# Kernel tuning notes

Hardware: AMD Instinct MI355X
Metric: run time of the kernel (lower is better)

## Reference

```python
import jax, jax.numpy as jnp
import numpy as np

B, S, D, H = 2, 2048, 1024, 16
HD = D // H  # head_dim = 64


def setup_inputs() -> dict:
    key = jax.random.key(0)
    ks = jax.random.split(key, 11)
    sc = 1.0 / np.sqrt(D)
    inp = {
        "query": jax.random.normal(ks[0], (B, S, D), jnp.float32),
        "key_": jax.random.normal(ks[1], (B, S, D), jnp.float32),
        "value": jax.random.normal(ks[2], (B, S, D), jnp.float32),
        "Wq": jax.random.normal(ks[3], (D, D), jnp.float32) * sc,
        "bq": jnp.zeros((D,), jnp.float32),
        "Wk": jax.random.normal(ks[4], (D, D), jnp.float32) * sc,
        "bk": jnp.zeros((D,), jnp.float32),
        "Wv": jax.random.normal(ks[5], (D, D), jnp.float32) * sc,
        "bv": jnp.zeros((D,), jnp.float32),
        "Wo": jax.random.normal(ks[6], (D, D), jnp.float32) * sc,
        "bo": jnp.zeros((D,), jnp.float32),
    }
    return inp


def _split_heads(x):
    # [B,S,D] -> [B,H,S,HD]
    return x.reshape(B, -1, H, HD).transpose(0, 2, 1, 3)


def reference(query, key_, value, Wq, bq, Wk, bk, Wv, bv, Wo, bo):
    q = _split_heads(query @ Wq.T + bq)
    k = _split_heads(key_ @ Wk.T + bk)
    v = _split_heads(value @ Wv.T + bv)
    scores = jnp.einsum("bhqd,bhkd->bhqk", q, k) / jnp.sqrt(jnp.float32(HD))
    attn = jax.nn.softmax(scores, axis=-1)  # dropout is identity in eval
    out = jnp.einsum("bhqk,bhkd->bhqd", attn, v)
    out = out.transpose(0, 2, 1, 3).reshape(B, -1, D)
    return out @ Wo.T + bo
```

## Files before the change

### kernel.cpp

```cpp
#include <hip/hip_runtime.h>
#include <hip/hip_bf16.h>
#include <stdint.h>

#define B_  2
#define S_  2048
#define D_  1024
#define H_  16
#define HD_ 64
#define M_  (B_*S_)

typedef __bf16 bf16x8 __attribute__((ext_vector_type(8)));
typedef __bf16 bf16x4 __attribute__((ext_vector_type(4)));
typedef short  s16x4  __attribute__((ext_vector_type(4)));
typedef float  f32x4  __attribute__((ext_vector_type(4)));
typedef unsigned int u32x4 __attribute__((ext_vector_type(4)));
typedef unsigned int u32x2 __attribute__((ext_vector_type(2)));
typedef unsigned short ushort_t;
typedef ushort_t u16x8 __attribute__((ext_vector_type(8)));

#define LOG2E 1.44269504088896f

#if __has_builtin(__builtin_amdgcn_exp2f)
#define EXP2(x) __builtin_amdgcn_exp2f(x)
#else
#define EXP2(x) exp2f(x)
#endif

__device__ __forceinline__ ushort_t f2bf(float f) {
    return __builtin_bit_cast(ushort_t, (__bf16)f);
}
__device__ __forceinline__ bf16x8 load_frag(const ushort_t* p) {
    u32x4 r = *reinterpret_cast<const u32x4*>(p);
    return __builtin_bit_cast(bf16x8, r);
}
__device__ __forceinline__ bf16x8 lds_frag(const ushort_t* p) {
    u32x4 r = *reinterpret_cast<const u32x4*>(p);
    return __builtin_bit_cast(bf16x8, r);
}
__device__ __forceinline__ bf16x4 lds_frag4(const ushort_t* p) {
    u32x2 r = *reinterpret_cast<const u32x2*>(p);
    return __builtin_bit_cast(bf16x4, r);
}
__device__ __forceinline__ void gld_lds16(const ushort_t* g, ushort_t* l) {
    __builtin_amdgcn_global_load_lds(
        (const __attribute__((address_space(1))) void*)g,
        (__attribute__((address_space(3))) void*)l, 16, 0, 0);
}

__device__ __forceinline__ f32x4 mfma16_bf16(bf16x4 a, bf16x4 b, f32x4 c) {
#if __has_builtin(__builtin_amdgcn_mfma_f32_16x16x16_bf16)
    return __builtin_amdgcn_mfma_f32_16x16x16_bf16(a, b, c, 0, 0, 0);
#elif __has_builtin(__builtin_amdgcn_mfma_f32_16x16x16bf16_1k)
    return __builtin_amdgcn_mfma_f32_16x16x16bf16_1k(
        __builtin_bit_cast(s16x4, a), __builtin_bit_cast(s16x4, b), c, 0, 0, 0);
#else
    f32x4 d;
    asm("v_mfma_f32_16x16x16_bf16 %0, %1, %2, %3"
        : "=v"(d) : "v"(a), "v"(b), "v"(c));
    return d;
#endif
}

__device__ __forceinline__ void cvt_body(const float* __restrict__ in,
                                         ushort_t* __restrict__ out, int i) {
    f32x4 v0 = *reinterpret_cast<const f32x4*>(in + i);
    f32x4 v1 = *reinterpret_cast<const f32x4*>(in + i + 4);
    u16x8 o;
#pragma unroll
    for (int j = 0; j < 4; ++j) { o[j] = f2bf(v0[j]); o[4 + j] = f2bf(v1[j]); }
    *reinterpret_cast<u16x8*>(out + i) = o;
}

__global__ __launch_bounds__(256) void cvt_all_kernel(
    const float* q, const float* k, const float* v,
    const float* fwq, const float* fwk, const float* fwv, const float* fwo,
    ushort_t* oq, ushort_t* ok, ushort_t* ov,
    ushort_t* owq, ushort_t* owk, ushort_t* owv, ushort_t* owo)
{
    const size_t T = (size_t)M_ * D_;
    const size_t U = (size_t)D_ * D_;
    const size_t idx = ((size_t)blockIdx.x * 256 + threadIdx.x) * 8;
    const float* in; ushort_t* out; size_t off;
    if (idx < 3 * T) {
        const size_t w = idx >> 22; off = idx & (T - 1);
        in  = (w == 0) ? q  : (w == 1) ? k  : v;
        out = (w == 0) ? oq : (w == 1) ? ok : ov;
    } else {
        const size_t r = idx - 3 * T;
        const size_t w = r >> 20; off = r & (U - 1);
        in  = (w == 0) ? fwq : (w == 1) ? fwk : (w == 2) ? fwv : fwo;
        out = (w == 0) ? owq : (w == 1) ? owk : (w == 2) ? owv : owo;
    }
    cvt_body(in, out, (int)off);
}

__device__ __forceinline__ void gemm_body(const ushort_t* __restrict__ X,
                                          const ushort_t* __restrict__ W,
                                          const float* __restrict__ bias,
                                          void* __restrict__ out, int mode)
{
    __shared__ ushort_t lA[128 * 32];
    __shared__ ushort_t lB[128 * 32];

    const int tid  = threadIdx.x;
    const int lane = tid & 63;
    const int wv   = tid >> 6;
    const int m0   = blockIdx.x * 128;
    const int n0   = blockIdx.y * 128;
    const int wr   = (wv >> 1) * 64;
    const int wc   = (wv & 1) * 64;
    const int l15  = lane & 15;
    const int lg   = lane >> 4;

    f32x4 acc[4][4];
#pragma unroll
    for (int i = 0; i < 4; ++i)
#pragma unroll
        for (int j = 0; j < 4; ++j) acc[i][j] = (f32x4){0.f, 0.f, 0.f, 0.f};

    const int srow = lane >> 2;
    const int skc  = ((lane & 3) ^ ((srow >> 1) & 3)) * 8;
    const int c0   = wv * 2, c1 = wv * 2 + 1;
    const size_t arow0 = (size_t)(m0 + c0 * 16 + srow) * D_ + skc;
    const size_t arow1 = (size_t)(m0 + c1 * 16 + srow) * D_ + skc;
    const size_t brow0 = (size_t)(n0 + c0 * 16 + srow) * D_ + skc;
    const size_t brow1 = (size_t)(n0 + c1 * 16 + srow) * D_ + skc;

    const int rchunk = (lg ^ ((l15 >> 1) & 3)) * 8;

    for (int kt = 0; kt < D_ / 32; ++kt) {
        const int k0 = kt * 32;
        gld_lds16(X + arow0 + k0, &lA[c0 * 512]);
        gld_lds16(X + arow1 + k0, &lA[c1 * 512]);
        gld_lds16(W + brow0 + k0, &lB[c0 * 512]);
        gld_lds16(W + brow1 + k0, &lB[c1 * 512]);
        __syncthreads();

        bf16x8 a[4], b[4];
#pragma unroll
        for (int i = 0; i < 4; ++i)
            a[i] = lds_frag(&lA[(wr + i * 16 + l15) * 32 + rchunk]);
#pragma unroll
        for (int j = 0; j < 4; ++j)
            b[j] = lds_frag(&lB[(wc + j * 16 + l15) * 32 + rchunk]);
#pragma unroll
        for (int i = 0; i < 4; ++i)
#pragma unroll
            for (int j = 0; j < 4; ++j)
                acc[i][j] = __builtin_amdgcn_mfma_f32_16x16x32_bf16(a[i], b[j], acc[i][j], 0, 0, 0);
        __syncthreads();
    }

#pragma unroll
    for (int i = 0; i < 4; ++i) {
#pragma unroll
        for (int j = 0; j < 4; ++j) {
            const int gcol = n0 + wc + j * 16 + l15;
            const float bv = bias[gcol];
#pragma unroll
            for (int r = 0; r < 4; ++r) {
                const int grow = m0 + wr + i * 16 + lg * 4 + r;
                float v = acc[i][j][r] + bv;
                if (mode == 0) v *= 0.125f * LOG2E;
                if (mode == 3) {
                    ((float*)out)[(size_t)grow * D_ + gcol] = v;
                } else {
                    const int b = grow >> 11, s = grow & (S_ - 1);
                    const int h = gcol >> 6,  hd = gcol & 63;
                    size_t addr;
                    if (mode == 2) addr = ((size_t)(b * H_ + h) * HD_ + hd) * S_ + s;
                    else           addr = ((size_t)(b * H_ + h) * S_ + s) * HD_ + hd;
                    ((ushort_t*)out)[addr] = f2bf(v);
                }
            }
        }
    }
}

__global__ __launch_bounds__(256) void qkv_kernel(
    const ushort_t* q_in, const ushort_t* k_in, const ushort_t* v_in,
    const ushort_t* Wq, const ushort_t* Wk, const ushort_t* Wv,
    const float* bq, const float* bk, const float* bv,
    ushort_t* qo, ushort_t* ko, ushort_t* vo)
{
    const int z = blockIdx.z;
    const ushort_t* X  = (z == 0) ? q_in : (z == 1) ? k_in : v_in;
    const ushort_t* W  = (z == 0) ? Wq   : (z == 1) ? Wk   : Wv;
    const float*    bs = (z == 0) ? bq   : (z == 1) ? bk   : bv;
    ushort_t*       o  = (z == 0) ? qo   : (z == 1) ? ko   : vo;
    gemm_body(X, W, bs, o, (z == 2) ? 2 : z);
}

__global__ __launch_bounds__(256) void oproj_kernel(
    const ushort_t* X, const ushort_t* W, const float* bias, float* out)
{
    gemm_body(X, W, bias, out, 3);
}

#define KVB 64
#define NT  (S_ / KVB)
#define SM_K0 0
#define SM_K1 4096
#define SM_V0 8192
#define SM_V1 12288
#define SM_TOT 17920

__global__ __launch_bounds__(512, 4) void attn_kernel(
    const ushort_t* __restrict__ Q, const ushort_t* __restrict__ K,
    const ushort_t* __restrict__ VT, ushort_t* __restrict__ O)
{
    __shared__ ushort_t smem[SM_TOT];

    const int lane = threadIdx.x & 63;
    const int wv   = threadIdx.x >> 6;
    const int wq   = wv & 3;
    const int wkv  = wv >> 2;
    const int bh   = blockIdx.x;
    const int qb   = blockIdx.y;
    const int qbase = qb * 128 + wq * 32;
    const int l15  = lane & 15;
    const int lg   = lane >> 4;

    const ushort_t* Qp = Q  + (size_t)bh * S_ * HD_;
    const ushort_t* Kp = K  + (size_t)bh * S_ * HD_;
    const ushort_t* Vp = VT + (size_t)bh * HD_ * S_;

    const int kr = threadIdx.x >> 3;
    const int kc = ((threadIdx.x & 7) ^ (kr & 7)) * 8;
    const int koff = threadIdx.x * 8;

    auto stage = [&](int tile, ushort_t* kdst, ushort_t* vdst) {
        gld_lds16(Kp + (size_t)(tile * KVB + kr) * HD_ + kc, kdst + koff);
        gld_lds16(Vp + (size_t)kr * S_ + tile * KVB + kc,    vdst + koff);
    };

    int offk[2][2];
#pragma unroll
    for (int j = 0; j < 2; ++j)
#pragma unroll
        for (int c = 0; c < 2; ++c)
            offk[j][c] = (wkv * 32 + j * 16 + l15) * 64 +
                         ((c * 32 + lg * 8) ^ ((l15 & 7) << 3));
    int offv[4][2];
#pragma unroll
    for (int dt = 0; dt < 4; ++dt)
#pragma unroll
        for (int j = 0; j < 2; ++j)
            offv[dt][j] = (dt * 16 + l15) * 64 +
                          (((wkv * 4 + j * 2 + (lg >> 1)) ^ (l15 & 7)) << 3) +
                          (lg & 1) * 4;

    bf16x8 aq[2][2];
#pragma unroll
    for (int qh = 0; qh < 2; ++qh)
#pragma unroll
        for (int c = 0; c < 2; ++c)
            aq[c][qh] = load_frag(Qp + (size_t)(qbase + qh * 16 + l15) * HD_ + c * 32 + lg * 8);

    f32x4 accO[4][2];
#pragma unroll
    for (int dt = 0; dt < 4; ++dt)
#pragma unroll
        for (int qh = 0; qh < 2; ++qh) accO[dt][qh] = (f32x4){0.f, 0.f, 0.f, 0.f};
    float lrun0 = 0.f, lrun1 = 0.f;

    stage(0, &smem[SM_K0], &smem[SM_V0]);

    for (int t = 0; t < NT; ++t) {
        const int cur = t & 1;
        const ushort_t* kb = cur ? &smem[SM_K1] : &smem[SM_K0];
        const ushort_t* vb = cur ? &smem[SM_V1] : &smem[SM_V0];

        __builtin_amdgcn_s_barrier();
        if (t + 1 < NT) {
            stage(t + 1, cur ? &smem[SM_K0] : &smem[SM_K1],
                          cur ? &smem[SM_V0] : &smem[SM_V1]);
            asm volatile("s_waitcnt vmcnt(2)" ::: "memory");
        } else {
            asm volatile("s_waitcnt vmcnt(0)" ::: "memory");
        }
        __builtin_amdgcn_s_barrier();
        __builtin_amdgcn_sched_barrier(0);

        f32x4 st[2][2];
#pragma unroll
        for (int j = 0; j < 2; ++j)
#pragma unroll
            for (int qh = 0; qh < 2; ++qh) st[j][qh] = (f32x4){0.f, 0.f, 0.f, 0.f};
        __builtin_amdgcn_s_setprio(1);
#pragma unroll
        for (int j = 0; j < 2; ++j) {
            bf16x8 k0 = lds_frag(&kb[offk[j][0]]);
            bf16x8 k1 = lds_frag(&kb[offk[j][1]]);
            st[j][0] = __builtin_amdgcn_mfma_f32_16x16x32_bf16(k0, aq[0][0], st[j][0], 0, 0, 0);
            st[j][0] = __builtin_amdgcn_mfma_f32_16x16x32_bf16(k1, aq[1][0], st[j][0], 0, 0, 0);
            st[j][1] = __builtin_amdgcn_mfma_f32_16x16x32_bf16(k0, aq[0][1], st[j][1], 0, 0, 0);
            st[j][1] = __builtin_amdgcn_mfma_f32_16x16x32_bf16(k1, aq[1][1], st[j][1], 0, 0, 0);
        }
        __builtin_amdgcn_s_setprio(0);

        bf16x4 pb[2][2];
#pragma unroll
        for (int qh = 0; qh < 2; ++qh) {
#pragma unroll
            for (int j = 0; j < 2; ++j) {
                float p0 = EXP2(st[j][qh][0]);
                float p1 = EXP2(st[j][qh][1]);
                float p2 = EXP2(st[j][qh][2]);
                float p3 = EXP2(st[j][qh][3]);
                u32x2 w;
                w[0] = (unsigned)f2bf(p0) | ((unsigned)f2bf(p1) << 16);
                w[1] = (unsigned)f2bf(p2) | ((unsigned)f2bf(p3) << 16);
                pb[j][qh] = __builtin_bit_cast(bf16x4, w);
                const float s = (p0 + p1) + (p2 + p3);
                if (qh == 0) lrun0 += s; else lrun1 += s;
            }
        }

        __builtin_amdgcn_s_setprio(1);
#pragma unroll
        for (int dt = 0; dt < 4; ++dt) {
#pragma unroll
            for (int j = 0; j < 2; ++j) {
                bf16x4 vf = lds_frag4(&vb[offv[dt][j]]);
                accO[dt][0] = mfma16_bf16(vf, pb[j][0], accO[dt][0]);
                accO[dt][1] = mfma16_bf16(vf, pb[j][1], accO[dt][1]);
            }
        }
        __builtin_amdgcn_s_setprio(0);
    }

    lrun0 += __shfl_xor(lrun0, 16);
    lrun0 += __shfl_xor(lrun0, 32);
    lrun1 += __shfl_xor(lrun1, 16);
    lrun1 += __shfl_xor(lrun1, 32);

    __syncthreads();
    float* cbuf = (float*)smem;

    if (wkv == 1) {
#pragma unroll
        for (int qh = 0; qh < 2; ++qh) {
            const int rowq = (wq * 2 + qh) * 16 + l15;
#pragma unroll
            for (int dt = 0; dt < 4; ++dt)
                *reinterpret_cast<f32x4*>(&cbuf[rowq * 68 + dt * 16 + lg * 4]) = accO[dt][qh];
        }
        if (lane < 16) {
            cbuf[128 * 68 + (wq * 2 + 0) * 16 + lane] = lrun0;
            cbuf[128 * 68 + (wq * 2 + 1) * 16 + lane] = lrun1;
        }
    }
    __syncthreads();

    if (wkv == 0) {
        const int b = bh >> 4, h = bh & 15;
#pragma unroll
        for (int qh = 0; qh < 2; ++qh) {
            const int rowq = (wq * 2 + qh) * 16 + l15;
            const float lsum = (qh == 0 ? lrun0 : lrun1) + cbuf[128 * 68 + rowq];
            const float inv = 1.0f / lsum;
            const size_t rowbase =
                (size_t)(b * S_ + qbase + qh * 16 + l15) * D_ + h * 64;
#pragma unroll
            for (int dt = 0; dt < 4; ++dt) {
                f32x4 part = *reinterpret_cast<f32x4*>(&cbuf[rowq * 68 + dt * 16 + lg * 4]);
                f32x4 tot  = accO[dt][qh] + part;
                u32x2 w;
                w[0] = (unsigned)f2bf(tot[0] * inv) | ((unsigned)f2bf(tot[1] * inv) << 16);
                w[1] = (unsigned)f2bf(tot[2] * inv) | ((unsigned)f2bf(tot[3] * inv) << 16);
                *reinterpret_cast<u32x2*>(&O[rowbase + dt * 16 + lg * 4]) = w;
            }
        }
    }
}

extern "C" void kernel_launch(void* const* d_in, const int* in_sizes, int n_in,
                              void* d_out, int out_size, void* d_ws, size_t ws_size,
                              hipStream_t stream)
{
    const float* query = (const float*)d_in[0];
    const float* key_  = (const float*)d_in[1];
    const float* value = (const float*)d_in[2];
    const float* Wq    = (const float*)d_in[3];
    const float* bq    = (const float*)d_in[4];
    const float* Wk    = (const float*)d_in[5];
    const float* bk    = (const float*)d_in[6];
    const float* Wv    = (const float*)d_in[7];
    const float* bv    = (const float*)d_in[8];
    const float* Wo    = (const float*)d_in[9];
    const float* bo    = (const float*)d_in[10];

    ushort_t* ws   = (ushort_t*)d_ws;
    const size_t T = (size_t)M_ * D_;
    const size_t U = (size_t)D_ * D_;
    ushort_t* xq  = ws;
    ushort_t* xk  = xq + T;
    ushort_t* xv  = xk + T;
    ushort_t* wq  = xv + T;
    ushort_t* wk  = wq + U;
    ushort_t* wv  = wk + U;
    ushort_t* wo  = wv + U;
    ushort_t* qws  = wo + U;
    ushort_t* kws  = qws + T;
    ushort_t* vtws = kws + T;
    ushort_t* aows = vtws + T;

    const int cvt_blocks = (int)((3 * T + 4 * U) / (256 * 8));
    cvt_all_kernel<<<cvt_blocks, 256, 0, stream>>>(
        query, key_, value, Wq, Wk, Wv, Wo,
        xq, xk, xv, wq, wk, wv, wo);

    qkv_kernel<<<dim3(32, 8, 3), 256, 0, stream>>>(
        xq, xk, xv, wq, wk, wv, bq, bk, bv, qws, kws, vtws);

    attn_kernel<<<dim3(32, 16), 512, 0, stream>>>(qws, kws, vtws, aows);

    oproj_kernel<<<dim3(32, 8, 1), 256, 0, stream>>>(
        aows, wo, bo, (float*)d_out);
}
```

Before: 124.3 us.

## Fuse fp32-to-bf16 conversion into GEMM tile loads and drop convert kernel

Removes the standalone conversion pass over inputs and weights. The projection GEMMs now load fp32 tiles into registers, prefetch the next tile, and convert to bf16 while storing to LDS. The attention output is written in fp32 and consumed directly by the output projection. This saves a launch and a full bf16 write/read round trip, but doubles the bytes each GEMM tile fetches and replaces the async direct-to-LDS loads with register staging.

After: 129.4 us. +4.1%, slower.

```diff
diff --git a/kernel.cpp b/kernel.cpp
--- a/kernel.cpp
+++ b/kernel.cpp
@@ -61,41 +61,8 @@
 #endif
 }
 
-__device__ __forceinline__ void cvt_body(const float* __restrict__ in,
-                                         ushort_t* __restrict__ out, int i) {
-    f32x4 v0 = *reinterpret_cast<const f32x4*>(in + i);
-    f32x4 v1 = *reinterpret_cast<const f32x4*>(in + i + 4);
-    u16x8 o;
-#pragma unroll
-    for (int j = 0; j < 4; ++j) { o[j] = f2bf(v0[j]); o[4 + j] = f2bf(v1[j]); }
-    *reinterpret_cast<u16x8*>(out + i) = o;
-}
-
-__global__ __launch_bounds__(256) void cvt_all_kernel(
-    const float* q, const float* k, const float* v,
-    const float* fwq, const float* fwk, const float* fwv, const float* fwo,
-    ushort_t* oq, ushort_t* ok, ushort_t* ov,
-    ushort_t* owq, ushort_t* owk, ushort_t* owv, ushort_t* owo)
-{
-    const size_t T = (size_t)M_ * D_;
-    const size_t U = (size_t)D_ * D_;
-    const size_t idx = ((size_t)blockIdx.x * 256 + threadIdx.x) * 8;
-    const float* in; ushort_t* out; size_t off;
-    if (idx < 3 * T) {
-        const size_t w = idx >> 22; off = idx & (T - 1);
-        in  = (w == 0) ? q  : (w == 1) ? k  : v;
-        out = (w == 0) ? oq : (w == 1) ? ok : ov;
-    } else {
-        const size_t r = idx - 3 * T;
-        const size_t w = r >> 20; off = r & (U - 1);
-        in  = (w == 0) ? fwq : (w == 1) ? fwk : (w == 2) ? fwv : fwo;
-        out = (w == 0) ? owq : (w == 1) ? owk : (w == 2) ? owv : owo;
-    }
-    cvt_body(in, out, (int)off);
-}
-
-__device__ __forceinline__ void gemm_body(const ushort_t* __restrict__ X,
-                                          const ushort_t* __restrict__ W,
+__device__ __forceinline__ void gemm_body(const float* __restrict__ X,
+                                          const float* __restrict__ W,
                                           const float* __restrict__ bias,
                                           void* __restrict__ out, int mode)
 {
@@ -118,23 +85,53 @@
 #pragma unroll
         for (int j = 0; j < 4; ++j) acc[i][j] = (f32x4){0.f, 0.f, 0.f, 0.f};
 
-    const int srow = lane >> 2;
-    const int skc  = ((lane & 3) ^ ((srow >> 1) & 3)) * 8;
-    const int c0   = wv * 2, c1 = wv * 2 + 1;
-    const size_t arow0 = (size_t)(m0 + c0 * 16 + srow) * D_ + skc;
-    const size_t arow1 = (size_t)(m0 + c1 * 16 + srow) * D_ + skc;
-    const size_t brow0 = (size_t)(n0 + c0 * 16 + srow) * D_ + skc;
-    const size_t brow1 = (size_t)(n0 + c1 * 16 + srow) * D_ + skc;
+    const int srow  = lane >> 2;
+    const int g4    = lane & 3;
+    const int slot8 = (g4 ^ ((srow >> 1) & 3)) * 8;
+    const int c0    = wv * 2, c1 = wv * 2 + 1;
+
+    const float* gsrc[4];
+    ushort_t*    ldst[4];
+    gsrc[0] = X + (size_t)(m0 + c0 * 16 + srow) * D_ + g4 * 8;
+    gsrc[1] = X + (size_t)(m0 + c1 * 16 + srow) * D_ + g4 * 8;
+    gsrc[2] = W + (size_t)(n0 + c0 * 16 + srow) * D_ + g4 * 8;
+    gsrc[3] = W + (size_t)(n0 + c1 * 16 + srow) * D_ + g4 * 8;
+    ldst[0] = &lA[(c0 * 16 + srow) * 32 + slot8];
+    ldst[1] = &lA[(c1 * 16 + srow) * 32 + slot8];
+    ldst[2] = &lB[(c0 * 16 + srow) * 32 + slot8];
+    ldst[3] = &lB[(c1 * 16 + srow) * 32 + slot8];
 
     const int rchunk = (lg ^ ((l15 >> 1) & 3)) * 8;
 
-    for (int kt = 0; kt < D_ / 32; ++kt) {
-        const int k0 = kt * 32;
-        gld_lds16(X + arow0 + k0, &lA[c0 * 512]);
-        gld_lds16(X + arow1 + k0, &lA[c1 * 512]);
-        gld_lds16(W + brow0 + k0, &lB[c0 * 512]);
-        gld_lds16(W + brow1 + k0, &lB[c1 * 512]);
+    f32x4 rg[4][2];
+#pragma unroll
+    for (int c = 0; c < 4; ++c) {
+        rg[c][0] = *reinterpret_cast<const f32x4*>(gsrc[c]);
+        rg[c][1] = *reinterpret_cast<const f32x4*>(gsrc[c] + 4);
+    }
+
+    const int NKT = D_ / 32;
+    for (int kt = 0; kt < NKT; ++kt) {
+#pragma unroll
+        for (int c = 0; c < 4; ++c) {
+            u16x8 o;
+#pragma unroll
+            for (int j = 0; j < 4; ++j) {
+                o[j]     = f2bf(rg[c][0][j]);
+                o[4 + j] = f2bf(rg[c][1][j]);
+            }
+            *reinterpret_cast<u16x8*>(ldst[c]) = o;
+        }
         __syncthreads();
+
+        if (kt + 1 < NKT) {
+            const int k1 = (kt + 1) * 32;
+#pragma unroll
+            for (int c = 0; c < 4; ++c) {
+                rg[c][0] = *reinterpret_cast<const f32x4*>(gsrc[c] + k1);
+                rg[c][1] = *reinterpret_cast<const f32x4*>(gsrc[c] + k1 + 4);
+            }
+        }
 
         bf16x8 a[4], b[4];
 #pragma unroll
@@ -177,22 +174,22 @@
     }
 }
 
-__global__ __launch_bounds__(256) void qkv_kernel(
-    const ushort_t* q_in, const ushort_t* k_in, const ushort_t* v_in,
-    const ushort_t* Wq, const ushort_t* Wk, const ushort_t* Wv,
+__global__ __launch_bounds__(256, 3) void qkv_kernel(
+    const float* q_in, const float* k_in, const float* v_in,
+    const float* Wq, const float* Wk, const float* Wv,
     const float* bq, const float* bk, const float* bv,
     ushort_t* qo, ushort_t* ko, ushort_t* vo)
 {
     const int z = blockIdx.z;
-    const ushort_t* X  = (z == 0) ? q_in : (z == 1) ? k_in : v_in;
-    const ushort_t* W  = (z == 0) ? Wq   : (z == 1) ? Wk   : Wv;
-    const float*    bs = (z == 0) ? bq   : (z == 1) ? bk   : bv;
-    ushort_t*       o  = (z == 0) ? qo   : (z == 1) ? ko   : vo;
+    const float* X  = (z == 0) ? q_in : (z == 1) ? k_in : v_in;
+    const float* W  = (z == 0) ? Wq   : (z == 1) ? Wk   : Wv;
+    const float* bs = (z == 0) ? bq   : (z == 1) ? bk   : bv;
+    ushort_t*    o  = (z == 0) ? qo   : (z == 1) ? ko   : vo;
     gemm_body(X, W, bs, o, (z == 2) ? 2 : z);
 }
 
-__global__ __launch_bounds__(256) void oproj_kernel(
-    const ushort_t* X, const ushort_t* W, const float* bias, float* out)
+__global__ __launch_bounds__(256, 3) void oproj_kernel(
+    const float* X, const float* W, const float* bias, float* out)
 {
     gemm_body(X, W, bias, out, 3);
 }
@@ -207,7 +204,7 @@
 
 __global__ __launch_bounds__(512, 4) void attn_kernel(
     const ushort_t* __restrict__ Q, const ushort_t* __restrict__ K,
-    const ushort_t* __restrict__ VT, ushort_t* __restrict__ O)
+    const ushort_t* __restrict__ VT, float* __restrict__ O)
 {
     __shared__ ushort_t smem[SM_TOT];
 
@@ -366,10 +363,8 @@
             for (int dt = 0; dt < 4; ++dt) {
                 f32x4 part = *reinterpret_cast<f32x4*>(&cbuf[rowq * 68 + dt * 16 + lg * 4]);
                 f32x4 tot  = accO[dt][qh] + part;
-                u32x2 w;
-                w[0] = (unsigned)f2bf(tot[0] * inv) | ((unsigned)f2bf(tot[1] * inv) << 16);
-                w[1] = (unsigned)f2bf(tot[2] * inv) | ((unsigned)f2bf(tot[3] * inv) << 16);
-                *reinterpret_cast<u32x2*>(&O[rowbase + dt * 16 + lg * 4]) = w;
+                tot[0] *= inv; tot[1] *= inv; tot[2] *= inv; tot[3] *= inv;
+                *reinterpret_cast<f32x4*>(&O[rowbase + dt * 16 + lg * 4]) = tot;
             }
         }
     }
@@ -393,29 +388,16 @@
 
     ushort_t* ws   = (ushort_t*)d_ws;
     const size_t T = (size_t)M_ * D_;
-    const size_t U = (size_t)D_ * D_;
-    ushort_t* xq  = ws;
-    ushort_t* xk  = xq + T;
-    ushort_t* xv  = xk + T;
-    ushort_t* wq  = xv + T;
-    ushort_t* wk  = wq + U;
-    ushort_t* wv  = wk + U;
-    ushort_t* wo  = wv + U;
-    ushort_t* qws  = wo + U;
+    ushort_t* qws  = ws;
     ushort_t* kws  = qws + T;
     ushort_t* vtws = kws + T;
-    ushort_t* aows = vtws + T;
-
-    const int cvt_blocks = (int)((3 * T + 4 * U) / (256 * 8));
-    cvt_all_kernel<<<cvt_blocks, 256, 0, stream>>>(
-        query, key_, value, Wq, Wk, Wv, Wo,
-        xq, xk, xv, wq, wk, wv, wo);
+    float*    aowsf = (float*)(ws + 3 * T);
 
     qkv_kernel<<<dim3(32, 8, 3), 256, 0, stream>>>(
-        xq, xk, xv, wq, wk, wv, bq, bk, bv, qws, kws, vtws);
-
-    attn_kernel<<<dim3(32, 16), 512, 0, stream>>>(qws, kws, vtws, aows);
+        query, key_, value, Wq, Wk, Wv, bq, bk, bv, qws, kws, vtws);
+
+    attn_kernel<<<dim3(32, 16), 512, 0, stream>>>(qws, kws, vtws, aowsf);
 
     oproj_kernel<<<dim3(32, 8, 1), 256, 0, stream>>>(
-        aows, wo, bo, (float*)d_out);
-}
+        aowsf, Wo, bo, (float*)d_out);
+}
```

## Halve attention block to 256 threads with 64 query rows and double grid

Applied to the files above, without the earlier changes.

The attention kernel now uses 4 waves (2 query waves × 2 KV-split waves) covering 64 query rows per block instead of 8 waves and 128 rows, and the grid doubles to 1024 blocks. Each thread now issues two K and two V async loads per tile, using pointer increments and buffer-pointer swaps instead of recomputed offsets. The aim is more blocks for load balancing across CUs and smaller blocks that may schedule more densely. In exchange, each K/V tile is reused by fewer queries, so total K/V traffic from global memory doubles. LDS shrinks slightly and the combine buffer is resized to match.

Measured after the change: 127.9 us. +2.9%, slower.

```diff
diff --git a/kernel.cpp b/kernel.cpp
--- a/kernel.cpp
+++ b/kernel.cpp
@@ -203,21 +203,22 @@
 #define SM_K1 4096
 #define SM_V0 8192
 #define SM_V1 12288
-#define SM_TOT 17920
-
-__global__ __launch_bounds__(512, 4) void attn_kernel(
+#define SM_TOT 16384
+
+__global__ __launch_bounds__(256, 4) void attn_kernel(
     const ushort_t* __restrict__ Q, const ushort_t* __restrict__ K,
     const ushort_t* __restrict__ VT, ushort_t* __restrict__ O)
 {
     __shared__ ushort_t smem[SM_TOT];
 
-    const int lane = threadIdx.x & 63;
-    const int wv   = threadIdx.x >> 6;
-    const int wq   = wv & 3;
-    const int wkv  = wv >> 2;
+    const int tid  = threadIdx.x;
+    const int lane = tid & 63;
+    const int wv   = tid >> 6;
+    const int wq   = wv & 1;
+    const int wkv  = wv >> 1;
     const int bh   = blockIdx.x;
     const int qb   = blockIdx.y;
-    const int qbase = qb * 128 + wq * 32;
+    const int qbase = qb * 64 + wq * 32;
     const int l15  = lane & 15;
     const int lg   = lane >> 4;
 
@@ -225,14 +226,13 @@
     const ushort_t* Kp = K  + (size_t)bh * S_ * HD_;
     const ushort_t* Vp = VT + (size_t)bh * HD_ * S_;
 
-    const int kr = threadIdx.x >> 3;
-    const int kc = ((threadIdx.x & 7) ^ (kr & 7)) * 8;
-    const int koff = threadIdx.x * 8;
-
-    auto stage = [&](int tile, ushort_t* kdst, ushort_t* vdst) {
-        gld_lds16(Kp + (size_t)(tile * KVB + kr) * HD_ + kc, kdst + koff);
-        gld_lds16(Vp + (size_t)kr * S_ + tile * KVB + kc,    vdst + koff);
-    };
+    const int m0s = tid, m1s = 256 + tid;
+    const int kr0 = m0s >> 3, kc0 = ((m0s & 7) ^ (kr0 & 7)) * 8;
+    const int kr1 = m1s >> 3, kc1 = ((m1s & 7) ^ (kr1 & 7)) * 8;
+    const ushort_t* kg0 = Kp + (size_t)kr0 * HD_ + kc0;
+    const ushort_t* kg1 = Kp + (size_t)kr1 * HD_ + kc1;
+    const ushort_t* vg0 = Vp + (size_t)kr0 * S_ + kc0;
+    const ushort_t* vg1 = Vp + (size_t)kr1 * S_ + kc1;
 
     int offk[2][2];
 #pragma unroll
@@ -264,18 +264,26 @@
         for (int qh = 0; qh < 2; ++qh) accO[dt][qh] = (f32x4){0.f, 0.f, 0.f, 0.f};
     float lrun0 = 0.f, lrun1 = 0.f;
 
-    stage(0, &smem[SM_K0], &smem[SM_V0]);
+    ushort_t* kcur = &smem[SM_K0];
+    ushort_t* knxt = &smem[SM_K1];
+    ushort_t* vcur = &smem[SM_V0];
+    ushort_t* vnxt = &smem[SM_V1];
+
+    gld_lds16(kg0, kcur + m0s * 8);
+    gld_lds16(kg1, kcur + m1s * 8);
+    gld_lds16(vg0, vcur + m0s * 8);
+    gld_lds16(vg1, vcur + m1s * 8);
+    kg0 += KVB * HD_; kg1 += KVB * HD_; vg0 += KVB; vg1 += KVB;
 
     for (int t = 0; t < NT; ++t) {
-        const int cur = t & 1;
-        const ushort_t* kb = cur ? &smem[SM_K1] : &smem[SM_K0];
-        const ushort_t* vb = cur ? &smem[SM_V1] : &smem[SM_V0];
-
         __builtin_amdgcn_s_barrier();
         if (t + 1 < NT) {
-            stage(t + 1, cur ? &smem[SM_K0] : &smem[SM_K1],
-                          cur ? &smem[SM_V0] : &smem[SM_V1]);
-            asm volatile("s_waitcnt vmcnt(2)" ::: "memory");
+            gld_lds16(kg0, knxt + m0s * 8);
+            gld_lds16(kg1, knxt + m1s * 8);
+            gld_lds16(vg0, vnxt + m0s * 8);
+            gld_lds16(vg1, vnxt + m1s * 8);
+            kg0 += KVB * HD_; kg1 += KVB * HD_; vg0 += KVB; vg1 += KVB;
+            asm volatile("s_waitcnt vmcnt(4)" ::: "memory");
         } else {
             asm volatile("s_waitcnt vmcnt(0)" ::: "memory");
         }
@@ -290,8 +298,8 @@
         __builtin_amdgcn_s_setprio(1);
 #pragma unroll
         for (int j = 0; j < 2; ++j) {
-            bf16x8 k0 = lds_frag(&kb[offk[j][0]]);
-            bf16x8 k1 = lds_frag(&kb[offk[j][1]]);
+            bf16x8 k0 = lds_frag(&kcur[offk[j][0]]);
+            bf16x8 k1 = lds_frag(&kcur[offk[j][1]]);
             st[j][0] = __builtin_amdgcn_mfma_f32_16x16x32_bf16(k0, aq[0][0], st[j][0], 0, 0, 0);
             st[j][0] = __builtin_amdgcn_mfma_f32_16x16x32_bf16(k1, aq[1][0], st[j][0], 0, 0, 0);
             st[j][1] = __builtin_amdgcn_mfma_f32_16x16x32_bf16(k0, aq[0][1], st[j][1], 0, 0, 0);
@@ -322,12 +330,15 @@
         for (int dt = 0; dt < 4; ++dt) {
 #pragma unroll
             for (int j = 0; j < 2; ++j) {
-                bf16x4 vf = lds_frag4(&vb[offv[dt][j]]);
+                bf16x4 vf = lds_frag4(&vcur[offv[dt][j]]);
                 accO[dt][0] = mfma16_bf16(vf, pb[j][0], accO[dt][0]);
                 accO[dt][1] = mfma16_bf16(vf, pb[j][1], accO[dt][1]);
             }
         }
         __builtin_amdgcn_s_setprio(0);
+
+        ushort_t* tk = kcur; kcur = knxt; knxt = tk;
+        ushort_t* tv = vcur; vcur = vnxt; vnxt = tv;
     }
 
     lrun0 += __shfl_xor(lrun0, 16);
@@ -347,8 +358,8 @@
                 *reinterpret_cast<f32x4*>(&cbuf[rowq * 68 + dt * 16 + lg * 4]) = accO[dt][qh];
         }
         if (lane < 16) {
-            cbuf[128 * 68 + (wq * 2 + 0) * 16 + lane] = lrun0;
-            cbuf[128 * 68 + (wq * 2 + 1) * 16 + lane] = lrun1;
+            cbuf[64 * 68 + (wq * 2 + 0) * 16 + lane] = lrun0;
+            cbuf[64 * 68 + (wq * 2 + 1) * 16 + lane] = lrun1;
         }
     }
     __syncthreads();
@@ -358,7 +369,7 @@
 #pragma unroll
         for (int qh = 0; qh < 2; ++qh) {
             const int rowq = (wq * 2 + qh) * 16 + l15;
-            const float lsum = (qh == 0 ? lrun0 : lrun1) + cbuf[128 * 68 + rowq];
+            const float lsum = (qh == 0 ? lrun0 : lrun1) + cbuf[64 * 68 + rowq];
             const float inv = 1.0f / lsum;
             const size_t rowbase =
                 (size_t)(b * S_ + qbase + qh * 16 + l15) * D_ + h * 64;
@@ -414,7 +425,7 @@
     qkv_kernel<<<dim3(32, 8, 3), 256, 0, stream>>>(
         xq, xk, xv, wq, wk, wv, bq, bk, bv, qws, kws, vtws);
 
-    attn_kernel<<<dim3(32, 16), 512, 0, stream>>>(qws, kws, vtws, aows);
+    attn_kernel<<<dim3(32, 32), 256, 0, stream>>>(qws, kws, vtws, aows);
 
     oproj_kernel<<<dim3(32, 8, 1), 256, 0, stream>>>(
         aows, wo, bo, (float*)d_out);
```

## Load K/V fragments directly from global into registers, drop LDS and KV split

Applied to the files above, without the earlier changes.

The attention kernel stops staging K/V tiles through shared memory with barriers. Each wave now loads its MFMA fragments straight from global memory into registers, double-buffered across 32-key steps. The two-wave KV split and its LDS reduction are removed, so each block is 4 waves that each walk the full sequence for 32 query rows. This cuts LDS traffic and barrier sync, but each wave now reads all of K/V itself with fewer waves in flight, so it leans on L2/L1 bandwidth and latency hiding.

Result: slower. 250.4 us (+101.4%).

```diff
diff --git a/kernel.cpp b/kernel.cpp
--- a/kernel.cpp
+++ b/kernel.cpp
@@ -33,13 +33,13 @@
     u32x4 r = *reinterpret_cast<const u32x4*>(p);
     return __builtin_bit_cast(bf16x8, r);
 }
+__device__ __forceinline__ bf16x4 load_frag4(const ushort_t* p) {
+    u32x2 r = *reinterpret_cast<const u32x2*>(p);
+    return __builtin_bit_cast(bf16x4, r);
+}
 __device__ __forceinline__ bf16x8 lds_frag(const ushort_t* p) {
     u32x4 r = *reinterpret_cast<const u32x4*>(p);
     return __builtin_bit_cast(bf16x8, r);
-}
-__device__ __forceinline__ bf16x4 lds_frag4(const ushort_t* p) {
-    u32x2 r = *reinterpret_cast<const u32x2*>(p);
-    return __builtin_bit_cast(bf16x4, r);
 }
 __device__ __forceinline__ void gld_lds16(const ushort_t* g, ushort_t* l) {
     __builtin_amdgcn_global_load_lds(
@@ -197,27 +197,23 @@
     gemm_body(X, W, bias, out, 3);
 }
 
-#define KVB 64
-#define NT  (S_ / KVB)
-#define SM_K0 0
-#define SM_K1 4096
-#define SM_V0 8192
-#define SM_V1 12288
-#define SM_TOT 17920
-
-__global__ __launch_bounds__(512, 4) void attn_kernel(
+#define KST 32
+#define NST (S_ / KST)
+
+struct KVFrag {
+    bf16x8 kf[2][2];
+    bf16x4 vf[4][2];
+};
+
+__global__ __launch_bounds__(256, 3) void attn_kernel(
     const ushort_t* __restrict__ Q, const ushort_t* __restrict__ K,
     const ushort_t* __restrict__ VT, ushort_t* __restrict__ O)
 {
-    __shared__ ushort_t smem[SM_TOT];
-
     const int lane = threadIdx.x & 63;
     const int wv   = threadIdx.x >> 6;
-    const int wq   = wv & 3;
-    const int wkv  = wv >> 2;
     const int bh   = blockIdx.x;
     const int qb   = blockIdx.y;
-    const int qbase = qb * 128 + wq * 32;
+    const int qbase = qb * 128 + wv * 32;
     const int l15  = lane & 15;
     const int lg   = lane >> 4;
 
@@ -225,30 +221,11 @@
     const ushort_t* Kp = K  + (size_t)bh * S_ * HD_;
     const ushort_t* Vp = VT + (size_t)bh * HD_ * S_;
 
-    const int kr = threadIdx.x >> 3;
-    const int kc = ((threadIdx.x & 7) ^ (kr & 7)) * 8;
-    const int koff = threadIdx.x * 8;
-
-    auto stage = [&](int tile, ushort_t* kdst, ushort_t* vdst) {
-        gld_lds16(Kp + (size_t)(tile * KVB + kr) * HD_ + kc, kdst + koff);
-        gld_lds16(Vp + (size_t)kr * S_ + tile * KVB + kc,    vdst + koff);
-    };
-
-    int offk[2][2];
-#pragma unroll
-    for (int j = 0; j < 2; ++j)
-#pragma unroll
-        for (int c = 0; c < 2; ++c)
-            offk[j][c] = (wkv * 32 + j * 16 + l15) * 64 +
-                         ((c * 32 + lg * 8) ^ ((l15 & 7) << 3));
-    int offv[4][2];
-#pragma unroll
-    for (int dt = 0; dt < 4; ++dt)
-#pragma unroll
-        for (int j = 0; j < 2; ++j)
-            offv[dt][j] = (dt * 16 + l15) * 64 +
-                          (((wkv * 4 + j * 2 + (lg >> 1)) ^ (l15 & 7)) << 3) +
-                          (lg & 1) * 4;
+    const ushort_t* kbase = Kp + (size_t)l15 * HD_ + lg * 8;
+    const ushort_t* vb0 = Vp + (size_t)(0 * 16 + l15) * S_ + lg * 4;
+    const ushort_t* vb1 = Vp + (size_t)(1 * 16 + l15) * S_ + lg * 4;
+    const ushort_t* vb2 = Vp + (size_t)(2 * 16 + l15) * S_ + lg * 4;
+    const ushort_t* vb3 = Vp + (size_t)(3 * 16 + l15) * S_ + lg * 4;
 
     bf16x8 aq[2][2];
 #pragma unroll
@@ -264,24 +241,23 @@
         for (int qh = 0; qh < 2; ++qh) accO[dt][qh] = (f32x4){0.f, 0.f, 0.f, 0.f};
     float lrun0 = 0.f, lrun1 = 0.f;
 
-    stage(0, &smem[SM_K0], &smem[SM_V0]);
-
-    for (int t = 0; t < NT; ++t) {
-        const int cur = t & 1;
-        const ushort_t* kb = cur ? &smem[SM_K1] : &smem[SM_K0];
-        const ushort_t* vb = cur ? &smem[SM_V1] : &smem[SM_V0];
-
-        __builtin_amdgcn_s_barrier();
-        if (t + 1 < NT) {
-            stage(t + 1, cur ? &smem[SM_K0] : &smem[SM_K1],
-                          cur ? &smem[SM_V0] : &smem[SM_V1]);
-            asm volatile("s_waitcnt vmcnt(2)" ::: "memory");
-        } else {
-            asm volatile("s_waitcnt vmcnt(0)" ::: "memory");
-        }
-        __builtin_amdgcn_s_barrier();
-        __builtin_amdgcn_sched_barrier(0);
-
+    KVFrag fA, fB;
+
+    auto load_step = [&](int s, KVFrag& dst) {
+        const ushort_t* kp = kbase + (size_t)s * (KST * HD_);
+#pragma unroll
+        for (int j = 0; j < 2; ++j)
+#pragma unroll
+            for (int c = 0; c < 2; ++c)
+                dst.kf[j][c] = load_frag(kp + j * 16 * HD_ + c * 32);
+        const int so = s * KST;
+        dst.vf[0][0] = load_frag4(vb0 + so);     dst.vf[0][1] = load_frag4(vb0 + so + 16);
+        dst.vf[1][0] = load_frag4(vb1 + so);     dst.vf[1][1] = load_frag4(vb1 + so + 16);
+        dst.vf[2][0] = load_frag4(vb2 + so);     dst.vf[2][1] = load_frag4(vb2 + so + 16);
+        dst.vf[3][0] = load_frag4(vb3 + so);     dst.vf[3][1] = load_frag4(vb3 + so + 16);
+    };
+
+    auto compute_step = [&](const KVFrag& src) {
         f32x4 st[2][2];
 #pragma unroll
         for (int j = 0; j < 2; ++j)
@@ -290,18 +266,16 @@
         __builtin_amdgcn_s_setprio(1);
 #pragma unroll
         for (int j = 0; j < 2; ++j) {
-            bf16x8 k0 = lds_frag(&kb[offk[j][0]]);
-            bf16x8 k1 = lds_frag(&kb[offk[j][1]]);
-            st[j][0] = __builtin_amdgcn_mfma_f32_16x16x32_bf16(k0, aq[0][0], st[j][0], 0, 0, 0);
-            st[j][0] = __builtin_amdgcn_mfma_f32_16x16x32_bf16(k1, aq[1][0], st[j][0], 0, 0, 0);
-            st[j][1] = __builtin_amdgcn_mfma_f32_16x16x32_bf16(k0, aq[0][1], st[j][1], 0, 0, 0);
-            st[j][1] = __builtin_amdgcn_mfma_f32_16x16x32_bf16(k1, aq[1][1], st[j][1], 0, 0, 0);
+            st[j][0] = __builtin_amdgcn_mfma_f32_16x16x32_bf16(src.kf[j][0], aq[0][0], st[j][0], 0, 0, 0);
+            st[j][0] = __builtin_amdgcn_mfma_f32_16x16x32_bf16(src.kf[j][1], aq[1][0], st[j][0], 0, 0, 0);
+            st[j][1] = __builtin_amdgcn_mfma_f32_16x16x32_bf16(src.kf[j][0], aq[0][1], st[j][1], 0, 0, 0);
+            st[j][1] = __builtin_amdgcn_mfma_f32_16x16x32_bf16(src.kf[j][1], aq[1][1], st[j][1], 0, 0, 0);
         }
         __builtin_amdgcn_s_setprio(0);
 
         bf16x4 pb[2][2];
 #pragma unroll
-        for (int qh = 0; qh < 2; ++qh) {
+        for (int qh = 0; qh < 2; ++qh)
 #pragma unroll
             for (int j = 0; j < 2; ++j) {
                 float p0 = EXP2(st[j][qh][0]);
@@ -315,62 +289,47 @@
                 const float s = (p0 + p1) + (p2 + p3);
                 if (qh == 0) lrun0 += s; else lrun1 += s;
             }
-        }
 
         __builtin_amdgcn_s_setprio(1);
 #pragma unroll
-        for (int dt = 0; dt < 4; ++dt) {
+        for (int dt = 0; dt < 4; ++dt)
 #pragma unroll
             for (int j = 0; j < 2; ++j) {
-                bf16x4 vf = lds_frag4(&vb[offv[dt][j]]);
-                accO[dt][0] = mfma16_bf16(vf, pb[j][0], accO[dt][0]);
-                accO[dt][1] = mfma16_bf16(vf, pb[j][1], accO[dt][1]);
+                accO[dt][0] = mfma16_bf16(src.vf[dt][j], pb[j][0], accO[dt][0]);
+                accO[dt][1] = mfma16_bf16(src.vf[dt][j], pb[j][1], accO[dt][1]);
             }
-        }
         __builtin_amdgcn_s_setprio(0);
+    };
+
+    load_step(0, fA);
+
+    for (int s = 0; s < NST; s += 2) {
+        load_step(s + 1, fB);
+        compute_step(fA);
+        if (s + 2 < NST) load_step(s + 2, fA);
+        compute_step(fB);
     }
 
     lrun0 += __shfl_xor(lrun0, 16);
     lrun0 += __shfl_xor(lrun0, 32);
     lrun1 += __shfl_xor(lrun1, 16);
     lrun1 += __shfl_xor(lrun1, 32);
-
-    __syncthreads();
-    float* cbuf = (float*)smem;
-
-    if (wkv == 1) {
-#pragma unroll
-        for (int qh = 0; qh < 2; ++qh) {
-            const int rowq = (wq * 2 + qh) * 16 + l15;
-#pragma unroll
-            for (int dt = 0; dt < 4; ++dt)
-                *reinterpret_cast<f32x4*>(&cbuf[rowq * 68 + dt * 16 + lg * 4]) = accO[dt][qh];
-        }
-        if (lane < 16) {
-            cbuf[128 * 68 + (wq * 2 + 0) * 16 + lane] = lrun0;
-            cbuf[128 * 68 + (wq * 2 + 1) * 16 + lane] = lrun1;
-        }
-    }
-    __syncthreads();
-
-    if (wkv == 0) {
-        const int b = bh >> 4, h = bh & 15;
-#pragma unroll
-        for (int qh = 0; qh < 2; ++qh) {
-            const int rowq = (wq * 2 + qh) * 16 + l15;
-            const float lsum = (qh == 0 ? lrun0 : lrun1) + cbuf[128 * 68 + rowq];
-            const float inv = 1.0f / lsum;
-            const size_t rowbase =
-                (size_t)(b * S_ + qbase + qh * 16 + l15) * D_ + h * 64;
-#pragma unroll
-            for (int dt = 0; dt < 4; ++dt) {
-                f32x4 part = *reinterpret_cast<f32x4*>(&cbuf[rowq * 68 + dt * 16 + lg * 4]);
-                f32x4 tot  = accO[dt][qh] + part;
-                u32x2 w;
-                w[0] = (unsigned)f2bf(tot[0] * inv) | ((unsigned)f2bf(tot[1] * inv) << 16);
-                w[1] = (unsigned)f2bf(tot[2] * inv) | ((unsigned)f2bf(tot[3] * inv) << 16);
-                *reinterpret_cast<u32x2*>(&O[rowbase + dt * 16 + lg * 4]) = w;
-            }
+    const float inv0 = 1.0f / lrun0;
+    const float inv1 = 1.0f / lrun1;
+
+    const int b = bh >> 4, h = bh & 15;
+#pragma unroll
+    for (int qh = 0; qh < 2; ++qh) {
+        const float inv = (qh == 0) ? inv0 : inv1;
+        const size_t rowbase =
+            (size_t)(b * S_ + qbase + qh * 16 + l15) * D_ + h * 64;
+#pragma unroll
+        for (int dt = 0; dt < 4; ++dt) {
+            const f32x4 t = accO[dt][qh];
+            u32x2 w;
+            w[0] = (unsigned)f2bf(t[0] * inv) | ((unsigned)f2bf(t[1] * inv) << 16);
+            w[1] = (unsigned)f2bf(t[2] * inv) | ((unsigned)f2bf(t[3] * inv) << 16);
+            *reinterpret_cast<u32x2*>(&O[rowbase + dt * 16 + lg * 4]) = w;
         }
     }
 }
@@ -414,7 +373,7 @@
     qkv_kernel<<<dim3(32, 8, 3), 256, 0, stream>>>(
         xq, xk, xv, wq, wk, wv, bq, bk, bv, qws, kws, vtws);
 
-    attn_kernel<<<dim3(32, 16), 512, 0, stream>>>(qws, kws, vtws, aows);
+    attn_kernel<<<dim3(32, 16), 256, 0, stream>>>(qws, kws, vtws, aows);
 
     oproj_kernel<<<dim3(32, 8, 1), 256, 0, stream>>>(
         aows, wo, bo, (float*)d_out);
```
